# Kernel optimization log

Measured on AMD Instinct MI355X. Metric: run time of the kernel, lower is better.

Reference implementation:

```python
import jax, jax.numpy as jnp
import numpy as np

# Mamba2 defaults (mamba-ssm): expand=2, d_state=128, d_conv=4, headdim=64, ngroups=1
D_MODEL = 1024
D_INNER = 2 * D_MODEL            # 2048
D_STATE = 128
D_CONV = 4
HEADDIM = 64
NHEADS = D_INNER // HEADDIM      # 32
CONV_DIM = D_INNER + 2 * D_STATE # 2304 (x, B, C go through conv)
D_IN_PROJ = 2 * D_INNER + 2 * D_STATE + NHEADS  # 4384 (z, xBC, dt)
LN_EPS = 1e-6


def setup_inputs() -> dict:
    key = jax.random.key(0)
    ks = jax.random.split(key, 12)
    B, L, D = 8, 1024, D_MODEL
    x = jax.random.normal(ks[0], (B, L, D), jnp.float32)
    t = jax.random.normal(ks[1], (B, D), jnp.float32)
    y = jax.random.normal(ks[2], (B, L, D), jnp.float32)
    # adaLN linear (zero-init in the module; use small random values for a non-trivial baseline)
    w_ada = jax.random.normal(ks[3], (D, 3 * D), jnp.float32) * 0.02
    b_ada = jax.random.normal(ks[4], (3 * D,), jnp.float32) * 0.02
    # Mamba2 params
    w_in = jax.random.normal(ks[5], (D, D_IN_PROJ), jnp.float32) * (D ** -0.5)
    conv_w = jax.random.normal(ks[6], (CONV_DIM, D_CONV), jnp.float32) * (D_CONV ** -0.5)
    conv_b = jnp.zeros((CONV_DIM,), jnp.float32)
    # dt_bias = softplus^{-1}(dt) with dt log-uniform in [1e-3, 1e-1]
    dt0 = jnp.exp(jax.random.uniform(ks[7], (NHEADS,)) * (np.log(0.1) - np.log(0.001)) + np.log(0.001))
    dt_bias = dt0 + jnp.log(-jnp.expm1(-dt0))
    A_log = jnp.log(jax.random.uniform(ks[8], (NHEADS,), minval=1.0, maxval=16.0))
    D_param = jnp.ones((NHEADS,), jnp.float32)
    w_out = jax.random.normal(ks[9], (D_INNER, D), jnp.float32) * (D_INNER ** -0.5)
    return {"x": x, "t": t, "y": y, "w_ada": w_ada, "b_ada": b_ada, "w_in": w_in,
            "conv_w": conv_w, "conv_b": conv_b, "dt_bias": dt_bias, "A_log": A_log,
            "D_param": D_param, "w_out": w_out}


def _layernorm(x):
    mu = jnp.mean(x, axis=-1, keepdims=True)
    var = jnp.mean(jnp.square(x - mu), axis=-1, keepdims=True)
    return (x - mu) / jnp.sqrt(var + LN_EPS)


def _mamba2(u, w_in, conv_w, conv_b, dt_bias, A_log, D_param, w_out):
    B, L, _ = u.shape
    zxbcdt = u @ w_in  # [B, L, D_IN_PROJ]
    z = zxbcdt[..., :D_INNER]
    xBC = zxbcdt[..., D_INNER:D_INNER + CONV_DIM]
    dt = zxbcdt[..., D_INNER + CONV_DIM:]
    # depthwise causal conv1d (kernel=4) + silu
    xp = jnp.pad(xBC, ((0, 0), (D_CONV - 1, 0), (0, 0)))
    conv = conv_b
    for k in range(D_CONV):
        conv = conv + conv_w[:, k] * xp[:, k:k + L, :]
    xBC = jax.nn.silu(conv)
    xh = xBC[..., :D_INNER].reshape(B, L, NHEADS, HEADDIM)
    Bm = xBC[..., D_INNER:D_INNER + D_STATE]  # [B, L, N] (ngroups=1)
    Cm = xBC[..., D_INNER + D_STATE:]         # [B, L, N]
    dt = jax.nn.softplus(dt + dt_bias)        # [B, L, H]
    A = -jnp.exp(A_log)                       # [H]
    dA = jnp.exp(dt * A)                      # [B, L, H]
    dtx = dt[..., None] * xh                  # [B, L, H, P]

    def step(h, inp):
        dA_t, dtx_t, B_t, C_t = inp
        # h: [B, H, P, N]
        h = h * dA_t[:, :, None, None] + dtx_t[..., None] * B_t[:, None, None, :]
        y_t = jnp.einsum('bhpn,bn->bhp', h, C_t)
        return h, y_t

    h0 = jnp.zeros((B, NHEADS, HEADDIM, D_STATE), u.dtype)
    xs = (jnp.moveaxis(dA, 1, 0), jnp.moveaxis(dtx, 1, 0),
          jnp.moveaxis(Bm, 1, 0), jnp.moveaxis(Cm, 1, 0))
    _, ys = jax.lax.scan(step, h0, xs)        # ys: [L, B, H, P]
    yv = jnp.moveaxis(ys, 0, 1) + D_param[None, None, :, None] * xh
    yv = yv.reshape(B, L, D_INNER) * jax.nn.silu(z)  # rmsnorm=False -> silu(z) gating
    return yv @ w_out


def reference(x, t, y, w_ada, b_ada, w_in, conv_w, conv_b, dt_bias, A_log, D_param, w_out):
    at = jax.nn.silu(t) @ w_ada + b_ada   # [B, 3D]
    ay = jax.nn.silu(y) @ w_ada + b_ada   # [B, L, 3D]
    sh_t, sc_t, g_t = jnp.split(at, 3, axis=1)
    sh_y, sc_y, g_y = jnp.split(ay, 3, axis=2)
    shift = sh_t[:, None, :] + sh_y
    scale = sc_t[:, None, :] + sc_y
    gate = g_t[:, None, :] + g_y
    mod = _layernorm(x) * (1 + scale) + shift
    return gate * _mamba2(mod, w_in, conv_w, conv_b, dt_bias, A_log, D_param, w_out) + x
```

## Files before the change

### kernel.cpp

```cpp
#include <hip/hip_runtime.h>

typedef float f32x4 __attribute__((ext_vector_type(4)));
typedef __bf16 bf16x8 __attribute__((ext_vector_type(8)));
typedef unsigned short ushort;
typedef ushort ushort8 __attribute__((ext_vector_type(8)));
typedef ushort ushort4v __attribute__((ext_vector_type(4)));

#define DM 1024
#define DI 2048
#define DSTATE 128
#define NH 32
#define HD 64
#define CONVDIM 2304
#define DPROJ 4384
#define ROWS 8192

__device__ __forceinline__ float bf2f(ushort u){
  union { unsigned int i; float f; } v; v.i = ((unsigned int)u)<<16; return v.f;
}
__device__ __forceinline__ ushort f2bf(float f){
  union { float f; unsigned int i; } v; v.f = f;
  unsigned int r = v.i + 0x7FFFu + ((v.i>>16)&1u);
  return (ushort)(r>>16);
}
__device__ __forceinline__ float siluf(float x){ return x / (1.f + __expf(-x)); }

__device__ __forceinline__ void gload16(const ushort* g, ushort* l){
  __builtin_amdgcn_global_load_lds(
      (const __attribute__((address_space(1))) void*)g,
      (__attribute__((address_space(3))) void*)l, 16, 0, 0);
}

__global__ __launch_bounds__(256) void k_silu_cast(const float* __restrict__ in,
                                                   ushort* __restrict__ out, int n){
  int i = (blockIdx.x*256 + threadIdx.x)*4;
  if (i >= n) return;
  float4 v = *(const float4*)(in + i);
  ushort4v o;
  o.x = f2bf(siluf(v.x)); o.y = f2bf(siluf(v.y));
  o.z = f2bf(siluf(v.z)); o.w = f2bf(siluf(v.w));
  *(ushort4v*)(out + i) = o;
}

__global__ __launch_bounds__(256) void k_transpose_cast(const float* __restrict__ in,
                                                        ushort* __restrict__ out,
                                                        int K, int N){
  __shared__ float tile[32][33];
  int n0 = blockIdx.x*32, k0 = blockIdx.y*32;
  int tx = threadIdx.x & 31, ty = threadIdx.x >> 5;
  for (int r = ty; r < 32; r += 8) tile[r][tx] = in[(size_t)(k0+r)*N + n0+tx];
  __syncthreads();
  for (int r = ty; r < 32; r += 8) out[(size_t)(n0+r)*K + k0+tx] = f2bf(tile[tx][r]);
}

__global__ __launch_bounds__(256) void k_at(const float* __restrict__ t,
                                            const float* __restrict__ w_ada,
                                            const float* __restrict__ b_ada,
                                            float* __restrict__ at){
  __shared__ float st[1024];
  int b = blockIdx.y;
  int col = blockIdx.x*256 + threadIdx.x;
  for (int i = threadIdx.x; i < 1024; i += 256) st[i] = siluf(t[b*1024 + i]);
  __syncthreads();
  float acc = 0.f;
  for (int k = 0; k < 1024; ++k) acc += st[k] * w_ada[(size_t)k*3072 + col];
  at[b*3072 + col] = acc + b_ada[col];
}

#define STG(Q, KT) do{ \
  gload16(pA0 + (size_t)(KT)*32, &sm[(Q)*8192 + (wave*2+0)*512]); \
  gload16(pA1 + (size_t)(KT)*32, &sm[(Q)*8192 + (wave*2+1)*512]); \
  gload16(pB0 + (size_t)(KT)*32, &sm[(Q)*8192 + 4096 + (wave*2+0)*512]); \
  gload16(pB1 + (size_t)(KT)*32, &sm[(Q)*8192 + 4096 + (wave*2+1)*512]); }while(0)

#define CMP(BOFF) do{ \
  bf16x8 af[4], bfr[4]; \
  _Pragma("unroll") \
  for (int m=0;m<4;m++) af[m]  = *(const bf16x8*)&sm[(BOFF) + (wr*64 + m*16 + l16)*32 + kbs]; \
  _Pragma("unroll") \
  for (int n=0;n<4;n++) bfr[n] = *(const bf16x8*)&sm[(BOFF) + 4096 + (wc*64 + n*16 + l16)*32 + kbs]; \
  __builtin_amdgcn_s_setprio(1); \
  _Pragma("unroll") \
  for (int m=0;m<4;m++) \
    _Pragma("unroll") \
    for (int n=0;n<4;n++) \
      acc[m][n] = __builtin_amdgcn_mfma_f32_16x16x32_bf16(af[m], bfr[n], acc[m][n], 0, 0, 0); \
  __builtin_amdgcn_s_setprio(0); }while(0)

#define BODY(Q, T) do{ \
  STG(((Q)+2)%3, (T)+2); \
  CMP((Q)*8192); \
  asm volatile("s_waitcnt vmcnt(4)" ::: "memory"); \
  __builtin_amdgcn_s_barrier(); \
  __builtin_amdgcn_sched_barrier(0); }while(0)

template<int EPI>
__global__ __launch_bounds__(256)
void k_gemm(const ushort* __restrict__ Ag, const ushort* __restrict__ Bt,
            ushort* __restrict__ Cb, ushort* __restrict__ Cb2, ushort* __restrict__ Cb3,
            float* __restrict__ Cf,
            int M, int N, int K, int nbn,
            const float* __restrict__ bias, const float* __restrict__ at,
            const ushort* __restrict__ gateM, const float* __restrict__ xres){
  __shared__ __align__(16) ushort sm[3*8192];
  const int tid  = threadIdx.x;
  const int wave = tid >> 6, lane = tid & 63;
  const int nwg = gridDim.x, bid0 = blockIdx.x;
  const int wg = (bid0 & 7)*(nwg >> 3) + (bid0 >> 3);
  const int pg = nbn << 3;
  const int g  = wg / pg;
  const int rem = wg - g*pg;
  const int bm = (g << 3) + (rem & 7);
  const int bn = rem >> 3;
  const int wr = wave >> 1, wc = wave & 1;
  const int l16 = lane & 15, kb = lane >> 4;
  const int arow0 = (wave*2+0)*16 + (lane>>2);
  const int arow1 = (wave*2+1)*16 + (lane>>2);
  const int kcs = (lane & 3) ^ ((lane>>3)&3);
  const int kbs = (kb ^ ((l16>>1)&3))*8;

  const ushort* pA0 = Ag + (size_t)(bm*128 + arow0)*K + kcs*8;
  const ushort* pA1 = Ag + (size_t)(bm*128 + arow1)*K + kcs*8;
  int br0 = bn*128 + arow0; if (br0 > N-1) br0 = N-1;
  int br1 = bn*128 + arow1; if (br1 > N-1) br1 = N-1;
  const ushort* pB0 = Bt + (size_t)br0*K + kcs*8;
  const ushort* pB1 = Bt + (size_t)br1*K + kcs*8;

  f32x4 acc[4][4];
#pragma unroll
  for (int m=0;m<4;m++)
#pragma unroll
    for (int n=0;n<4;n++) acc[m][n] = (f32x4){0.f,0.f,0.f,0.f};

  const int NT = K >> 5;
  const int NB = NT - 2;

  STG(0, 0); STG(1, 1);
  asm volatile("s_waitcnt vmcnt(4)" ::: "memory");
  __builtin_amdgcn_s_barrier();
  __builtin_amdgcn_sched_barrier(0);

  int T = 0;
  for (; T + 3 <= NB; T += 3){
    BODY(0, T); BODY(1, T+1); BODY(2, T+2);
  }
  if (NB - T >= 1) BODY(0, T);
  if (NB - T >= 2) BODY(1, T+1);

  {
    const int qa = NB % 3, qb = (NB + 1) % 3;
    CMP(qa*8192);
    asm volatile("s_waitcnt vmcnt(0)" ::: "memory");
    __builtin_amdgcn_s_barrier();
    __builtin_amdgcn_sched_barrier(0);
    CMP(qb*8192);
  }

#pragma unroll
  for (int m=0;m<4;m++){
    int grow_base = bm*128 + wr*64 + m*16 + (lane>>4)*4;
#pragma unroll
    for (int n=0;n<4;n++){
      int gcol = bn*128 + wc*64 + n*16 + l16;
      if (EPI == 0){
        if (gcol < N){
#pragma unroll
          for (int r=0;r<4;r++){
            int row = grow_base + r;
            float v = acc[m][n][r];
            if (gcol < 2048)      Cb [(size_t)row*2048 + gcol] = f2bf(v);
            else if (gcol < 4352) Cb2[(size_t)row*2304 + (gcol-2048)] = f2bf(v);
            else                  Cb3[(size_t)row*32   + (gcol-4352)] = f2bf(v);
          }
        }
      } else if (EPI == 1){
        float bv = bias[gcol];
#pragma unroll
        for (int r=0;r<4;r++){
          int row = grow_base + r;
          float v = acc[m][n][r] + bv + at[(row>>10)*3072 + gcol];
          if (gcol < 2048) Cb [(size_t)row*2048 + gcol] = f2bf(v);
          else             Cb2[(size_t)row*1024 + (gcol - 2048)] = f2bf(v);
        }
      } else {
#pragma unroll
        for (int r=0;r<4;r++){
          int row = grow_base + r;
          float g2 = bf2f(gateM[(size_t)row*1024 + gcol]);
          Cf[(size_t)row*1024 + gcol] = g2*acc[m][n][r] + xres[(size_t)row*1024 + gcol];
        }
      }
    }
  }
}

__global__ __launch_bounds__(256) void k_lnmod(const float* __restrict__ x,
                                               const ushort* __restrict__ Mss,
                                               ushort* __restrict__ mod){
  int row = blockIdx.x;
  const float* xr = x + (size_t)row*1024;
  float v[4]; float s = 0.f, s2 = 0.f;
#pragma unroll
  for (int j=0;j<4;j++){ v[j] = xr[threadIdx.x + j*256]; s += v[j]; s2 += v[j]*v[j]; }
#pragma unroll
  for (int o=32;o>0;o>>=1){ s += __shfl_down(s,o); s2 += __shfl_down(s2,o); }
  __shared__ float ls[4], ls2[4];
  int wv = threadIdx.x >> 6;
  if ((threadIdx.x & 63) == 0){ ls[wv] = s; ls2[wv] = s2; }
  __syncthreads();
  s  = ls[0]+ls[1]+ls[2]+ls[3];
  s2 = ls2[0]+ls2[1]+ls2[2]+ls2[3];
  float mu = s * (1.f/1024.f);
  float var = s2 * (1.f/1024.f) - mu*mu;
  float rstd = rsqrtf(var + 1e-6f);
  const ushort* Mr = Mss + (size_t)row*2048;
#pragma unroll
  for (int j=0;j<4;j++){
    int d = threadIdx.x + j*256;
    float sc = bf2f(Mr[1024 + d]);
    float sh = bf2f(Mr[d]);
    mod[(size_t)row*1024 + d] = f2bf((v[j]-mu)*rstd*(1.f+sc) + sh);
  }
}

__global__ __launch_bounds__(256) void k_conv(const ushort* __restrict__ xbc,
                                              const float* __restrict__ conv_w,
                                              const float* __restrict__ conv_b,
                                              ushort* __restrict__ co){
  int ch  = blockIdx.x*256 + threadIdx.x;
  int row = blockIdx.y;
  int l = row & 1023, b = row >> 10;
  float acc = conv_b[ch];
#pragma unroll
  for (int k=0;k<4;k++){
    int ll = l - 3 + k;
    if (ll >= 0) acc += conv_w[ch*4 + k] * bf2f(xbc[(size_t)(b*1024 + ll)*CONVDIM + ch]);
  }
  co[(size_t)row*CONVDIM + ch] = f2bf(siluf(acc));
}

__global__ __launch_bounds__(256) void k_transT(const ushort* __restrict__ co,
                                                ushort* __restrict__ xhT,
                                                ushort* __restrict__ BTg){
  __shared__ ushort tile[64*72];
  const int c0 = blockIdx.x*64, l0 = blockIdx.y*64, b = blockIdx.z;
  const int tid = threadIdx.x;
  for (int q = tid; q < 512; q += 256){
    int r = q >> 3, cc = q & 7;
    ushort8 v = *(const ushort8*)(co + (size_t)(b*1024 + l0 + r)*CONVDIM + c0 + cc*8);
    *(ushort8*)&tile[r*72 + cc*8] = v;
  }
  __syncthreads();
  for (int q = tid; q < 1024; q += 256){
    int oc = q >> 4, lc = (q & 15)*4;
    ushort4v o;
#pragma unroll
    for (int j = 0; j < 4; ++j) o[j] = tile[(lc + j)*72 + oc];
    int ccol = c0 + oc;
    ushort* out = (ccol < 2048) ? (xhT + (size_t)(b*2048 + ccol)*1024)
                                : (BTg + (size_t)(b*128 + (ccol - 2048))*1024);
    *(ushort4v*)(out + l0 + lc) = o;
  }
}

__global__ __launch_bounds__(256) void k_chunkstate(
    const ushort* __restrict__ xhT, const ushort* __restrict__ BTg,
    const ushort* __restrict__ dtc,
    const float* __restrict__ dt_bias, const float* __restrict__ A_log,
    ushort* __restrict__ Sc, float* __restrict__ Dcb){
  __shared__ __align__(16) ushort sXG[64*128];
  __shared__ __align__(16) ushort sBT[128*128];
  __shared__ float sG[128];
  const int bid = blockIdx.x;
  const int h = bid & 31, bc = bid >> 5, b = bc >> 3, c = bc & 7;
  const int tid = threadIdx.x, wave = tid >> 6, lane = tid & 63;
  const int l16 = lane & 15, l4 = lane >> 4;
  const int sci = (b*32 + h)*8 + c;
  {
    const ushort* src = BTg + (size_t)(b*128)*1024 + c*128;
    for (int i2 = 0; i2 < 8; ++i2){
      int itg = wave*8 + i2;
      int r = itg*4 + l4;
      int cc = l16 ^ (r & 7);
      gload16(src + (size_t)r*1024 + cc*8, &sBT[itg*512]);
    }
  }
  const float Ah = -__expf(A_log[h]);
  if (wave == 0){
    const int row0 = b*1024 + c*128;
    float bi = dt_bias[h];
    float d0 = bf2f(dtc[(size_t)(row0 + 2*lane    )*32 + h]) + bi;
    float d1 = bf2f(dtc[(size_t)(row0 + 2*lane + 1)*32 + h]) + bi;
    d0 = (d0 > 20.f) ? d0 : log1pf(__expf(d0));
    d1 = (d1 > 20.f) ? d1 : log1pf(__expf(d1));
    float p = d0 + d1;
#pragma unroll
    for (int o = 1; o < 64; o <<= 1){
      float tp = __shfl_up(p, o);
      if (lane >= o) p += tp;
    }
    float cs127 = __shfl(p, 63);
    sG[2*lane    ] = __expf(Ah*(cs127 - (p - d1))) * d0;
    sG[2*lane + 1] = __expf(Ah*(cs127 - p)) * d1;
    if (lane == 0) Dcb[sci] = __expf(Ah*cs127);
  }
  __syncthreads();
  {
    const ushort* xsrc = xhT + (size_t)(b*2048 + h*64)*1024 + c*128;
    for (int q = tid; q < 1024; q += 256){
      int r = q >> 4, cc = q & 15;
      ushort8 v = *(const ushort8*)(xsrc + (size_t)r*1024 + cc*8);
      ushort8 o;
#pragma unroll
      for (int j = 0; j < 8; ++j) o[j] = f2bf(bf2f(v[j]) * sG[cc*8 + j]);
      *(ushort8*)&sXG[r*128 + ((cc ^ (r & 7))*8)] = o;
    }
  }
  __syncthreads();
  f32x4 acc[4][2];
#pragma unroll
  for (int m=0;m<4;m++)
#pragma unroll
    for (int nf=0;nf<2;nf++) acc[m][nf] = (f32x4){0.f,0.f,0.f,0.f};
  for (int ks = 0; ks < 4; ++ks){
    bf16x8 av[4], bv[2];
#pragma unroll
    for (int m = 0; m < 4; ++m){
      int rp = m*16 + l16;
      av[m] = *(const bf16x8*)&sXG[rp*128 + (((ks*4 + l4) ^ (rp & 7))*8)];
    }
#pragma unroll
    for (int nf = 0; nf < 2; ++nf){
      int rn = wave*32 + nf*16 + l16;
      bv[nf] = *(const bf16x8*)&sBT[rn*128 + (((ks*4 + l4) ^ (rn & 7))*8)];
    }
#pragma unroll
    for (int m = 0; m < 4; ++m)
#pragma unroll
      for (int nf = 0; nf < 2; ++nf)
        acc[m][nf] = __builtin_amdgcn_mfma_f32_16x16x32_bf16(av[m], bv[nf], acc[m][nf], 0, 0, 0);
  }
  const size_t base = (size_t)sci * 8192;
#pragma unroll
  for (int m = 0; m < 4; ++m)
#pragma unroll
    for (int nf = 0; nf < 2; ++nf)
#pragma unroll
      for (int r = 0; r < 4; ++r){
        int p = m*16 + l4*4 + r;
        int n = wave*32 + nf*16 + l16;
        Sc[base + p*128 + n] = f2bf(acc[m][nf][r]);
      }
}

__global__ __launch_bounds__(256) void k_chunkscan(ushort* __restrict__ Sc,
                                                   const float* __restrict__ Dcb){
  size_t idx = (size_t)blockIdx.x*256 + threadIdx.x;
  int bh = (int)(idx >> 13);
  int pn = (int)(idx & 8191);
  float hv = 0.f;
  for (int c = 0; c < 8; ++c){
    size_t o = (size_t)(bh*8 + c)*8192 + pn;
    float s = bf2f(Sc[o]);
    float dc = Dcb[bh*8 + c];
    Sc[o] = f2bf(hv);
    hv = hv*dc + s;
  }
}

__global__ __launch_bounds__(256, 2) void k_ssd(
    const ushort* __restrict__ co, const ushort* __restrict__ zz,
    const ushort* __restrict__ dtc, const ushort* __restrict__ xhT,
    const ushort* __restrict__ Hin,
    const float* __restrict__ dt_bias, const float* __restrict__ A_log,
    const float* __restrict__ D_param,
    ushort* __restrict__ yv){
  __shared__ __align__(16) ushort sC [128*128];
  __shared__ __align__(16) ushort sBP[128*128];
  __shared__ float csv[128], dtv[128];
  const int bid = blockIdx.x;
  const int h = bid & 31, bc = bid >> 5, b = bc >> 3, c = bc & 7;
  const int tid = threadIdx.x, wave = tid >> 6, lane = tid & 63;
  const int l16 = lane & 15, l4 = lane >> 4;
  const int wr = wave >> 1, wc = wave & 1;
  const int row0 = b*1024 + c*128;
  const ushort* cbase = co + (size_t)row0*CONVDIM;
  for (int i2 = 0; i2 < 8; ++i2){
    int itg = wave*8 + i2;
    int r = itg*4 + l4;
    int cc = l16 ^ (r & 7);
    gload16(cbase + (size_t)r*CONVDIM + 2176 + cc*8, &sC [itg*512]);
    gload16(cbase + (size_t)r*CONVDIM + 2048 + cc*8, &sBP[itg*512]);
  }
  bf16x8 xbr[2][4], hbr[2][4];
  {
    const size_t hbase = (size_t)((b*32 + h)*8 + c)*8192;
#pragma unroll
    for (int n = 0; n < 2; ++n){
      const int rp = wc*32 + n*16 + l16;
      const ushort* xrow = xhT + (size_t)(b*2048 + h*64 + rp)*1024 + c*128;
      const ushort* hrow = Hin + hbase + (size_t)rp*128;
#pragma unroll
      for (int ks = 0; ks < 4; ++ks){
        xbr[n][ks] = *(const bf16x8*)(xrow + (ks*4 + l4)*8);
        hbr[n][ks] = *(const bf16x8*)(hrow + (ks*4 + l4)*8);
      }
    }
  }
  const float Ah = -__expf(A_log[h]);
  if (wave == 0){
    float bi = dt_bias[h];
    float d0 = bf2f(dtc[(size_t)(row0 + 2*lane    )*32 + h]) + bi;
    float d1 = bf2f(dtc[(size_t)(row0 + 2*lane + 1)*32 + h]) + bi;
    d0 = (d0 > 20.f) ? d0 : log1pf(__expf(d0));
    d1 = (d1 > 20.f) ? d1 : log1pf(__expf(d1));
    float p = d0 + d1;
#pragma unroll
    for (int o = 1; o < 64; o <<= 1){
      float tp = __shfl_up(p, o);
      if (lane >= o) p += tp;
    }
    csv[2*lane    ] = p - d1;
    csv[2*lane + 1] = p;
    dtv[2*lane    ] = d0;
    dtv[2*lane + 1] = d1;
  }
  __syncthreads();
  f32x4 acc[4][4];
#pragma unroll
  for (int m=0;m<4;m++)
#pragma unroll
    for (int n=0;n<4;n++) acc[m][n] = (f32x4){0.f,0.f,0.f,0.f};
  for (int ks = 0; ks < 4; ++ks){
    bf16x8 av[4], bv[4];
#pragma unroll
    for (int m = 0; m < 4; ++m){
      int ri = wr*64 + m*16 + l16;
      av[m] = *(const bf16x8*)&sC[ri*128 + (((ks*4 + l4) ^ (ri & 7))*8)];
    }
#pragma unroll
    for (int n = 0; n < 4; ++n){
      int rs = wc*64 + n*16 + l16;
      bv[n] = *(const bf16x8*)&sBP[rs*128 + (((ks*4 + l4) ^ (rs & 7))*8)];
    }
#pragma unroll
    for (int m = 0; m < 4; ++m)
#pragma unroll
      for (int n = 0; n < 4; ++n)
        acc[m][n] = __builtin_amdgcn_mfma_f32_16x16x32_bf16(av[m], bv[n], acc[m][n], 0, 0, 0);
  }
  __syncthreads();
  const float Dp = D_param[h];
#pragma unroll
  for (int m = 0; m < 4; ++m){
#pragma unroll
    for (int r = 0; r < 4; ++r){
      int i = wr*64 + m*16 + l4*4 + r;
      float ci = csv[i];
#pragma unroll
      for (int n = 0; n < 4; ++n){
        int s = wc*64 + n*16 + l16;
        float e = __expf(Ah*(ci - csv[s]));
        float v = (i >= s) ? acc[m][n][r]*e*dtv[s] : 0.f;
        if (i == s) v += Dp;
        sBP[i*128 + (s ^ ((i & 7)<<3))] = f2bf(v);
      }
    }
  }
  __syncthreads();
  f32x4 accY[4][2], accI[4][2];
#pragma unroll
  for (int m=0;m<4;m++)
#pragma unroll
    for (int n=0;n<2;n++){ accY[m][n] = (f32x4){0.f,0.f,0.f,0.f}; accI[m][n] = (f32x4){0.f,0.f,0.f,0.f}; }
#pragma unroll
  for (int ks = 0; ks < 4; ++ks){
    bf16x8 pa[4], ca[4];
#pragma unroll
    for (int m = 0; m < 4; ++m){
      int ri = wr*64 + m*16 + l16;
      int off = ((ks*4 + l4) ^ (ri & 7))*8;
      pa[m] = *(const bf16x8*)&sBP[ri*128 + off];
      ca[m] = *(const bf16x8*)&sC [ri*128 + off];
    }
#pragma unroll
    for (int m = 0; m < 4; ++m)
#pragma unroll
      for (int n = 0; n < 2; ++n){
        accY[m][n] = __builtin_amdgcn_mfma_f32_16x16x32_bf16(pa[m], xbr[n][ks], accY[m][n], 0, 0, 0);
        accI[m][n] = __builtin_amdgcn_mfma_f32_16x16x32_bf16(ca[m], hbr[n][ks], accI[m][n], 0, 0, 0);
      }
  }
#pragma unroll
  for (int m = 0; m < 4; ++m){
#pragma unroll
    for (int r = 0; r < 4; ++r){
      int i = wr*64 + m*16 + l4*4 + r;
      float Ei = __expf(Ah*csv[i]);
      int grow = row0 + i;
#pragma unroll
      for (int n = 0; n < 2; ++n){
        int p = wc*32 + n*16 + l16;
        float yvl = accY[m][n][r] + Ei*accI[m][n][r];
        float z = bf2f(zz[(size_t)grow*2048 + h*64 + p]);
        yv[(size_t)grow*DI + h*64 + p] = f2bf(yvl * siluf(z));
      }
    }
  }
}

extern "C" void kernel_launch(void* const* d_in, const int* in_sizes, int n_in,
                              void* d_out, int out_size, void* d_ws, size_t ws_size,
                              hipStream_t stream){
  const float* x       = (const float*)d_in[0];
  const float* t       = (const float*)d_in[1];
  const float* y       = (const float*)d_in[2];
  const float* w_ada   = (const float*)d_in[3];
  const float* b_ada   = (const float*)d_in[4];
  const float* w_in    = (const float*)d_in[5];
  const float* conv_w  = (const float*)d_in[6];
  const float* conv_b  = (const float*)d_in[7];
  const float* dt_bias = (const float*)d_in[8];
  const float* A_log   = (const float*)d_in[9];
  const float* D_param = (const float*)d_in[10];
  const float* w_out   = (const float*)d_in[11];

  char* w = (char*)d_ws;
  size_t off = 0;
  auto alloc = [&](size_t bytes)->char*{
    char* p = w + off; off += (bytes + 255) & ~(size_t)255; return p;
  };
  ushort* zz    = (ushort*)alloc((size_t)ROWS*2048*2);
  ushort* xbc   = (ushort*)alloc((size_t)ROWS*CONVDIM*2);
  ushort* dtc   = (ushort*)alloc((size_t)ROWS*32*2);
  ushort* co    = (ushort*)alloc((size_t)ROWS*CONVDIM*2);
  ushort* Mss   = (ushort*)alloc((size_t)ROWS*2048*2);
  ushort* Mg    = (ushort*)alloc((size_t)ROWS*1024*2);
  ushort* yv    = (ushort*)alloc((size_t)ROWS*DI*2);
  ushort* woutT = (ushort*)alloc(1024ull*2048*2);
  ushort* waT   = (ushort*)alloc(3072ull*1024*2);
  ushort* winT  = (ushort*)alloc(4608ull*1024*2);
  float*  atb   = (float*) alloc(8ull*3072*4);
  ushort* Ya    = (ushort*)alloc((size_t)ROWS*1024*2);
  ushort* BTg   = (ushort*)alloc((size_t)8*128*1024*2);
  float*  Dcb   = (float*) alloc(2048ull*4);
  ushort* xhT   = xbc;
  ushort* Sc    = Mss;

  k_silu_cast<<<dim3(ROWS*1024/(256*4)), 256, 0, stream>>>(y, Ya, ROWS*1024);
  k_transpose_cast<<<dim3(96,32),  256, 0, stream>>>(w_ada, waT,  1024, 3072);
  k_transpose_cast<<<dim3(137,32), 256, 0, stream>>>(w_in,  winT, 1024, 4384);
  k_transpose_cast<<<dim3(32,64),  256, 0, stream>>>(w_out, woutT, 2048, 1024);
  k_at<<<dim3(12,8), 256, 0, stream>>>(t, w_ada, b_ada, atb);
  k_gemm<1><<<dim3(1536), 256, 0, stream>>>(Ya, waT, Mss, Mg, nullptr, nullptr, ROWS, 3072, 1024, 24,
                                            b_ada, atb, nullptr, nullptr);
  k_lnmod<<<dim3(ROWS), 256, 0, stream>>>(x, Mss, Ya);
  k_gemm<0><<<dim3(2240), 256, 0, stream>>>(Ya, winT, zz, xbc, dtc, nullptr, ROWS, DPROJ, 1024, 35,
                                            nullptr, nullptr, nullptr, nullptr);
  k_conv<<<dim3(9,ROWS), 256, 0, stream>>>(xbc, conv_w, conv_b, co);
  k_transT<<<dim3(34,16,8), 256, 0, stream>>>(co, xhT, BTg);
  k_chunkstate<<<dim3(2048), 256, 0, stream>>>(xhT, BTg, dtc, dt_bias, A_log, Sc, Dcb);
  k_chunkscan<<<dim3(8192), 256, 0, stream>>>(Sc, Dcb);
  k_ssd<<<dim3(2048), 256, 0, stream>>>(co, zz, dtc, xhT, Sc, dt_bias, A_log, D_param, yv);
  k_gemm<2><<<dim3(512), 256, 0, stream>>>(yv, woutT, nullptr, nullptr, nullptr, (float*)d_out,
                                           ROWS, 1024, 2048, 8, nullptr, nullptr, Mg, x);
}
```

Measured before the change: 486.9 us.

## Enlarge GEMM tiles to 256x128 with 8 waves and fuse conv with transpose

The GEMM kernel moves to 512-thread blocks computing 256x128 output tiles, so each B tile is shared across twice as many rows. The block-swizzle grouping and launch grids are halved to match, and the shared-memory stages grow to 72 KB in total. The depthwise conv and the transpose are merged into one kernel that stages a halo'd input tile in LDS. It writes the transposed x/B outputs directly and writes the row-major conv output only for the channels that need it, which removes one full pass over the conv activations. The buffer aliases for xhT and Sc are swapped to fit the new data flow. The trade-offs are lower occupancy from the larger tiles and LDS use, and a higher risk of aliasing mistakes.

```diff
diff --git a/kernel.cpp b/kernel.cpp
--- a/kernel.cpp
+++ b/kernel.cpp
@@ -68,17 +68,16 @@
 }
 
 #define STG(Q, KT) do{ \
-  gload16(pA0 + (size_t)(KT)*32, &sm[(Q)*8192 + (wave*2+0)*512]); \
-  gload16(pA1 + (size_t)(KT)*32, &sm[(Q)*8192 + (wave*2+1)*512]); \
-  gload16(pB0 + (size_t)(KT)*32, &sm[(Q)*8192 + 4096 + (wave*2+0)*512]); \
-  gload16(pB1 + (size_t)(KT)*32, &sm[(Q)*8192 + 4096 + (wave*2+1)*512]); }while(0)
+  gload16(pA0 + (size_t)(KT)*32, &sm[(Q)*12288 + (wave*2+0)*512]); \
+  gload16(pA1 + (size_t)(KT)*32, &sm[(Q)*12288 + (wave*2+1)*512]); \
+  gload16(pB0 + (size_t)(KT)*32, &sm[(Q)*12288 + 8192 + wave*512]); }while(0)
 
 #define CMP(BOFF) do{ \
   bf16x8 af[4], bfr[4]; \
   _Pragma("unroll") \
   for (int m=0;m<4;m++) af[m]  = *(const bf16x8*)&sm[(BOFF) + (wr*64 + m*16 + l16)*32 + kbs]; \
   _Pragma("unroll") \
-  for (int n=0;n<4;n++) bfr[n] = *(const bf16x8*)&sm[(BOFF) + 4096 + (wc*64 + n*16 + l16)*32 + kbs]; \
+  for (int n=0;n<4;n++) bfr[n] = *(const bf16x8*)&sm[(BOFF) + 8192 + (wc*64 + n*16 + l16)*32 + kbs]; \
   __builtin_amdgcn_s_setprio(1); \
   _Pragma("unroll") \
   for (int m=0;m<4;m++) \
@@ -89,42 +88,41 @@
 
 #define BODY(Q, T) do{ \
   STG(((Q)+2)%3, (T)+2); \
-  CMP((Q)*8192); \
-  asm volatile("s_waitcnt vmcnt(4)" ::: "memory"); \
+  CMP((Q)*12288); \
+  asm volatile("s_waitcnt vmcnt(3)" ::: "memory"); \
   __builtin_amdgcn_s_barrier(); \
   __builtin_amdgcn_sched_barrier(0); }while(0)
 
 template<int EPI>
-__global__ __launch_bounds__(256)
+__global__ __launch_bounds__(512)
 void k_gemm(const ushort* __restrict__ Ag, const ushort* __restrict__ Bt,
             ushort* __restrict__ Cb, ushort* __restrict__ Cb2, ushort* __restrict__ Cb3,
             float* __restrict__ Cf,
             int M, int N, int K, int nbn,
             const float* __restrict__ bias, const float* __restrict__ at,
             const ushort* __restrict__ gateM, const float* __restrict__ xres){
-  __shared__ __align__(16) ushort sm[3*8192];
+  __shared__ __align__(16) ushort sm[3*12288];
   const int tid  = threadIdx.x;
   const int wave = tid >> 6, lane = tid & 63;
   const int nwg = gridDim.x, bid0 = blockIdx.x;
   const int wg = (bid0 & 7)*(nwg >> 3) + (bid0 >> 3);
-  const int pg = nbn << 3;
+  const int pg = nbn << 2;
   const int g  = wg / pg;
   const int rem = wg - g*pg;
-  const int bm = (g << 3) + (rem & 7);
-  const int bn = rem >> 3;
+  const int bm = (g << 2) + (rem & 3);
+  const int bn = rem >> 2;
   const int wr = wave >> 1, wc = wave & 1;
   const int l16 = lane & 15, kb = lane >> 4;
   const int arow0 = (wave*2+0)*16 + (lane>>2);
   const int arow1 = (wave*2+1)*16 + (lane>>2);
+  const int brow  = wave*16 + (lane>>2);
   const int kcs = (lane & 3) ^ ((lane>>3)&3);
   const int kbs = (kb ^ ((l16>>1)&3))*8;
 
-  const ushort* pA0 = Ag + (size_t)(bm*128 + arow0)*K + kcs*8;
-  const ushort* pA1 = Ag + (size_t)(bm*128 + arow1)*K + kcs*8;
-  int br0 = bn*128 + arow0; if (br0 > N-1) br0 = N-1;
-  int br1 = bn*128 + arow1; if (br1 > N-1) br1 = N-1;
+  const ushort* pA0 = Ag + (size_t)(bm*256 + arow0)*K + kcs*8;
+  const ushort* pA1 = Ag + (size_t)(bm*256 + arow1)*K + kcs*8;
+  int br0 = bn*128 + brow; if (br0 > N-1) br0 = N-1;
   const ushort* pB0 = Bt + (size_t)br0*K + kcs*8;
-  const ushort* pB1 = Bt + (size_t)br1*K + kcs*8;
 
   f32x4 acc[4][4];
 #pragma unroll
@@ -136,7 +134,7 @@
   const int NB = NT - 2;
 
   STG(0, 0); STG(1, 1);
-  asm volatile("s_waitcnt vmcnt(4)" ::: "memory");
+  asm volatile("s_waitcnt vmcnt(3)" ::: "memory");
   __builtin_amdgcn_s_barrier();
   __builtin_amdgcn_sched_barrier(0);
 
@@ -149,16 +147,16 @@
 
   {
     const int qa = NB % 3, qb = (NB + 1) % 3;
-    CMP(qa*8192);
+    CMP(qa*12288);
     asm volatile("s_waitcnt vmcnt(0)" ::: "memory");
     __builtin_amdgcn_s_barrier();
     __builtin_amdgcn_sched_barrier(0);
-    CMP(qb*8192);
+    CMP(qb*12288);
   }
 
 #pragma unroll
   for (int m=0;m<4;m++){
-    int grow_base = bm*128 + wr*64 + m*16 + (lane>>4)*4;
+    int grow_base = bm*256 + wr*64 + m*16 + (lane>>4)*4;
 #pragma unroll
     for (int n=0;n<4;n++){
       int gcol = bn*128 + wc*64 + n*16 + l16;
@@ -223,43 +221,60 @@
   }
 }
 
-__global__ __launch_bounds__(256) void k_conv(const ushort* __restrict__ xbc,
-                                              const float* __restrict__ conv_w,
-                                              const float* __restrict__ conv_b,
-                                              ushort* __restrict__ co){
-  int ch  = blockIdx.x*256 + threadIdx.x;
-  int row = blockIdx.y;
-  int l = row & 1023, b = row >> 10;
-  float acc = conv_b[ch];
-#pragma unroll
-  for (int k=0;k<4;k++){
-    int ll = l - 3 + k;
-    if (ll >= 0) acc += conv_w[ch*4 + k] * bf2f(xbc[(size_t)(b*1024 + ll)*CONVDIM + ch]);
-  }
-  co[(size_t)row*CONVDIM + ch] = f2bf(siluf(acc));
-}
-
-__global__ __launch_bounds__(256) void k_transT(const ushort* __restrict__ co,
-                                                ushort* __restrict__ xhT,
-                                                ushort* __restrict__ BTg){
-  __shared__ ushort tile[64*72];
-  const int c0 = blockIdx.x*64, l0 = blockIdx.y*64, b = blockIdx.z;
+__global__ __launch_bounds__(256) void k_convT(const ushort* __restrict__ xbc,
+                                               const float* __restrict__ conv_w,
+                                               const float* __restrict__ conv_b,
+                                               ushort* __restrict__ co,
+                                               ushort* __restrict__ xhT,
+                                               ushort* __restrict__ BTg){
+  __shared__ ushort lin[67*64];
+  __shared__ __align__(16) ushort outb[64*76];
+  const int cb = blockIdx.x, lb = blockIdx.y, b = blockIdx.z;
+  const int ch0 = cb*64, l0 = lb*64;
   const int tid = threadIdx.x;
-  for (int q = tid; q < 512; q += 256){
-    int r = q >> 3, cc = q & 7;
-    ushort8 v = *(const ushort8*)(co + (size_t)(b*1024 + l0 + r)*CONVDIM + c0 + cc*8);
-    *(ushort8*)&tile[r*72 + cc*8] = v;
-  }
-  __syncthreads();
-  for (int q = tid; q < 1024; q += 256){
-    int oc = q >> 4, lc = (q & 15)*4;
-    ushort4v o;
-#pragma unroll
-    for (int j = 0; j < 4; ++j) o[j] = tile[(lc + j)*72 + oc];
-    int ccol = c0 + oc;
-    ushort* out = (ccol < 2048) ? (xhT + (size_t)(b*2048 + ccol)*1024)
-                                : (BTg + (size_t)(b*128 + (ccol - 2048))*1024);
-    *(ushort4v*)(out + l0 + lc) = o;
+  for (int q = tid; q < 67*8; q += 256){
+    int r = q >> 3, c8 = q & 7;
+    int l = l0 - 3 + r;
+    ushort8 v = {0,0,0,0,0,0,0,0};
+    if (l >= 0) v = *(const ushort8*)(xbc + (size_t)(b*1024 + l)*CONVDIM + ch0 + c8*8);
+    *(ushort8*)&lin[r*64 + c8*8] = v;
+  }
+  __syncthreads();
+  const int ch = tid & 63, lg = tid >> 6;
+  const int chg = ch0 + ch;
+  const float w0 = conv_w[chg*4+0], w1 = conv_w[chg*4+1];
+  const float w2 = conv_w[chg*4+2], w3 = conv_w[chg*4+3];
+  const float cbv = conv_b[chg];
+  __align__(16) ushort o[16];
+#pragma unroll
+  for (int j = 0; j < 16; ++j){
+    int r = lg*16 + j;
+    float a = cbv + w0*bf2f(lin[r*64+ch])     + w1*bf2f(lin[(r+1)*64+ch])
+                  + w2*bf2f(lin[(r+2)*64+ch]) + w3*bf2f(lin[(r+3)*64+ch]);
+    o[j] = f2bf(siluf(a));
+  }
+  if (cb < 34){
+    *(ushort8*)&outb[ch*76 + lg*16]     = *(ushort8*)&o[0];
+    *(ushort8*)&outb[ch*76 + lg*16 + 8] = *(ushort8*)&o[8];
+    __syncthreads();
+    int row = tid >> 2, seg = tid & 3;
+    ushort8 v0 = *(ushort8*)&outb[row*76 + seg*16];
+    ushort8 v1 = *(ushort8*)&outb[row*76 + seg*16 + 8];
+    ushort* dst = (cb < 32)
+      ? (xhT + (size_t)(b*2048 + ch0 + row)*1024 + l0 + seg*16)
+      : (BTg + (size_t)(b*128 + (ch0 - 2048) + row)*1024 + l0 + seg*16);
+    *(ushort8*)dst = v0; *(ushort8*)(dst+8) = v1;
+  }
+  if (cb >= 32){
+    __syncthreads();
+#pragma unroll
+    for (int j = 0; j < 16; ++j) outb[(lg*16+j)*76 + ch] = o[j];
+    __syncthreads();
+    int l = tid >> 2, seg = tid & 3;
+    ushort8 v0 = *(ushort8*)&outb[l*76 + seg*16];
+    ushort8 v1 = *(ushort8*)&outb[l*76 + seg*16 + 8];
+    ushort* dst = co + (size_t)(b*1024 + l0 + l)*CONVDIM + ch0 + seg*16;
+    *(ushort8*)dst = v0; *(ushort8*)(dst+8) = v1;
   }
 }
 
@@ -544,24 +559,23 @@
   ushort* Ya    = (ushort*)alloc((size_t)ROWS*1024*2);
   ushort* BTg   = (ushort*)alloc((size_t)8*128*1024*2);
   float*  Dcb   = (float*) alloc(2048ull*4);
-  ushort* xhT   = xbc;
-  ushort* Sc    = Mss;
+  ushort* xhT   = Mss;
+  ushort* Sc    = xbc;
 
   k_silu_cast<<<dim3(ROWS*1024/(256*4)), 256, 0, stream>>>(y, Ya, ROWS*1024);
   k_transpose_cast<<<dim3(96,32),  256, 0, stream>>>(w_ada, waT,  1024, 3072);
   k_transpose_cast<<<dim3(137,32), 256, 0, stream>>>(w_in,  winT, 1024, 4384);
   k_transpose_cast<<<dim3(32,64),  256, 0, stream>>>(w_out, woutT, 2048, 1024);
   k_at<<<dim3(12,8), 256, 0, stream>>>(t, w_ada, b_ada, atb);
-  k_gemm<1><<<dim3(1536), 256, 0, stream>>>(Ya, waT, Mss, Mg, nullptr, nullptr, ROWS, 3072, 1024, 24,
-                                            b_ada, atb, nullptr, nullptr);
+  k_gemm<1><<<dim3(768), 512, 0, stream>>>(Ya, waT, Mss, Mg, nullptr, nullptr, ROWS, 3072, 1024, 24,
+                                           b_ada, atb, nullptr, nullptr);
   k_lnmod<<<dim3(ROWS), 256, 0, stream>>>(x, Mss, Ya);
-  k_gemm<0><<<dim3(2240), 256, 0, stream>>>(Ya, winT, zz, xbc, dtc, nullptr, ROWS, DPROJ, 1024, 35,
+  k_gemm<0><<<dim3(1120), 512, 0, stream>>>(Ya, winT, zz, xbc, dtc, nullptr, ROWS, DPROJ, 1024, 35,
                                             nullptr, nullptr, nullptr, nullptr);
-  k_conv<<<dim3(9,ROWS), 256, 0, stream>>>(xbc, conv_w, conv_b, co);
-  k_transT<<<dim3(34,16,8), 256, 0, stream>>>(co, xhT, BTg);
+  k_convT<<<dim3(36,16,8), 256, 0, stream>>>(xbc, conv_w, conv_b, co, xhT, BTg);
   k_chunkstate<<<dim3(2048), 256, 0, stream>>>(xhT, BTg, dtc, dt_bias, A_log, Sc, Dcb);
   k_chunkscan<<<dim3(8192), 256, 0, stream>>>(Sc, Dcb);
   k_ssd<<<dim3(2048), 256, 0, stream>>>(co, zz, dtc, xhT, Sc, dt_bias, A_log, D_param, yv);
-  k_gemm<2><<<dim3(512), 256, 0, stream>>>(yv, woutT, nullptr, nullptr, nullptr, (float*)d_out,
+  k_gemm<2><<<dim3(256), 512, 0, stream>>>(yv, woutT, nullptr, nullptr, nullptr, (float*)d_out,
                                            ROWS, 1024, 2048, 8, nullptr, nullptr, Mg, x);
 }
```

Result: faster. 421.4 us (-13.5%).
